# Kernel tuning notes

Hardware: AMD Instinct MI355X
Metric: run time of the kernel (lower is better)

The kernel has to match this reference:

```python
import jax, jax.numpy as jnp
import numpy as np


def setup_inputs() -> dict:
    key = jax.random.key(0)
    k1, k2 = jax.random.split(key)
    B, C, LIN = 8, 128, 65536
    K, LOUT = 9, 16384
    x = jax.random.normal(k1, (B, C, LIN), dtype=jnp.float32)
    neighbours = jax.random.randint(k2, (K, LOUT), 0, LIN, dtype=jnp.int64)
    return {"x": x, "neighbours": neighbours}


def reference(x, neighbours):
    # x: (B, C, locs_in); neighbours: (k, locs_out)
    # gather -> (B, C, k, locs_out), max over k axis -> (B, C, locs_out)
    gathered = x[:, :, neighbours]
    return jnp.max(gathered, axis=-2)
```

## Files before the change

kernel.cpp:

```cpp
#include <hip/hip_runtime.h>
#include <hip/hip_fp16.h>


#define B_DIM 8
#define C_DIM 128
#define LIN 65536
#define K_DIM 9
#define LOUT 16384
#define BC 1024
#define LTILE 16
#define BCCHUNK 256

__global__ __launch_bounds__(256) void transpose_to_half(
    const float4* __restrict__ in4, __half* __restrict__ outh)
{
    __shared__ float tile[64][65];
    const int c0 = blockIdx.x * 64;
    const int r0 = blockIdx.y * 64;
    const int tx = threadIdx.x;
    const int ty = threadIdx.y;

#pragma unroll
    for (int i = 0; i < 4; ++i) {
        const int r = ty + 16 * i;
        const float4 v = in4[(size_t)(r0 + r) * (LIN / 4) + (c0 / 4) + tx];
        tile[r][4 * tx + 0] = v.x;
        tile[r][4 * tx + 1] = v.y;
        tile[r][4 * tx + 2] = v.z;
        tile[r][4 * tx + 3] = v.w;
    }
    __syncthreads();
#pragma unroll
    for (int i = 0; i < 4; ++i) {
        const int c = ty + 16 * i;
        const __half h0 = __float2half_rn(tile[4 * tx + 0][c]);
        const __half h1 = __float2half_rn(tile[4 * tx + 1][c]);
        const __half h2 = __float2half_rn(tile[4 * tx + 2][c]);
        const __half h3 = __float2half_rn(tile[4 * tx + 3][c]);
        ushort4 w;
        w.x = __half_as_ushort(h0);
        w.y = __half_as_ushort(h1);
        w.z = __half_as_ushort(h2);
        w.w = __half_as_ushort(h3);
        *(ushort4*)(outh + (size_t)(c0 + c) * BC + r0 + 4 * tx) = w;
    }
}

__global__ __launch_bounds__(256) void gather_max_half(
    const __half* __restrict__ xTh,
    const int* __restrict__ nbr,
    float* __restrict__ out)
{
    __shared__ float tile[LTILE][BCCHUNK + 4];
    __shared__ int sidx[K_DIM][LTILE];
    const int tid = threadIdx.x;
    const int l0 = blockIdx.x * LTILE;
    const int bc0 = blockIdx.y * BCCHUNK;

    if (tid < K_DIM * LTILE) {
        const int k = tid / LTILE, li = tid % LTILE;
        sidx[k][li] = nbr[k * LOUT + l0 + li];
    }
    __syncthreads();

    const int h = tid & 31;
    const int lgrp = tid >> 5;

#pragma unroll
    for (int j = 0; j < 2; ++j) {
        const int lidx = j * 8 + lgrp;
        float acc[8];
#pragma unroll
        for (int e = 0; e < 8; ++e) acc[e] = -INFINITY;
#pragma unroll
        for (int k = 0; k < K_DIM; ++k) {
            const int id = sidx[k][lidx];
            const float4 raw = *(const float4*)(xTh + (size_t)id * BC + bc0 + 8 * h);
            const __half2* hp = (const __half2*)&raw;
#pragma unroll
            for (int q = 0; q < 4; ++q) {
                const float2 f = __half22float2(hp[q]);
                acc[2 * q]     = fmaxf(acc[2 * q], f.x);
                acc[2 * q + 1] = fmaxf(acc[2 * q + 1], f.y);
            }
        }
        *(float4*)&tile[lidx][8 * h]     = make_float4(acc[0], acc[1], acc[2], acc[3]);
        *(float4*)&tile[lidx][8 * h + 4] = make_float4(acc[4], acc[5], acc[6], acc[7]);
    }
    __syncthreads();

    float* orow = out + (size_t)(bc0 + tid) * LOUT + l0;
#pragma unroll
    for (int j2 = 0; j2 < 4; ++j2) {
        float4 w;
        w.x = tile[4 * j2 + 0][tid];
        w.y = tile[4 * j2 + 1][tid];
        w.z = tile[4 * j2 + 2][tid];
        w.w = tile[4 * j2 + 3][tid];
        *(float4*)(orow + 4 * j2) = w;
    }
}

__global__ __launch_bounds__(256) void pool_gather_max_direct(
    const float* __restrict__ x, const int* __restrict__ nbr, float* __restrict__ out)
{
    const int l = blockIdx.x * 256 + threadIdx.x;
    const int bc0 = blockIdx.y * 8;
    int idx[K_DIM];
#pragma unroll
    for (int k = 0; k < K_DIM; ++k) idx[k] = nbr[k * LOUT + l];
#pragma unroll
    for (int r = 0; r < 8; ++r) {
        const float* __restrict__ xrow = x + (size_t)(bc0 + r) * LIN;
        float m = -INFINITY;
#pragma unroll
        for (int k = 0; k < K_DIM; ++k) m = fmaxf(m, xrow[idx[k]]);
        out[(size_t)(bc0 + r) * LOUT + l] = m;
    }
}

extern "C" void kernel_launch(void* const* d_in, const int* in_sizes, int n_in,
                              void* d_out, int out_size, void* d_ws, size_t ws_size,
                              hipStream_t stream) {
    const float* x   = (const float*)d_in[0];
    const int*   nbr = (const int*)d_in[1];
    float*       out = (float*)d_out;

    const size_t xTh_bytes = (size_t)LIN * BC * sizeof(__half);

    if (ws_size < xTh_bytes) {
        dim3 grid(LOUT / 256, BC / 8);
        pool_gather_max_direct<<<grid, dim3(256), 0, stream>>>(x, nbr, out);
        return;
    }

    __half* xTh = (__half*)d_ws;

    {
        dim3 grid(LIN / 64, BC / 64);
        transpose_to_half<<<grid, dim3(16, 16), 0, stream>>>((const float4*)x, xTh);
    }
    {
        dim3 grid(LOUT / LTILE, BC / BCCHUNK);
        gather_max_half<<<grid, dim3(256), 0, stream>>>(xTh, nbr, out);
    }
}
```

Before: 445.9 us.

## Fuse fp16 conversion and gather-max into per-row kernel using LDS-resident rows

Replaces the global transpose-to-fp16 plus gather kernel with one kernel where each block loads a full (b,c) input row, converts it to fp16 in 128 KB of shared memory, and performs the K-way gather-max from LDS. This removes the intermediate transposed workspace write and read and the scattered global gathers. In exchange, occupancy drops to one large block per CU, load and compute phases do not overlap, and random LDS accesses may bank-conflict. The neighbour indices are re-read by every block, and the low-workspace fallback path is removed.

```diff
diff --git a/kernel.cpp b/kernel.cpp
--- a/kernel.cpp
+++ b/kernel.cpp
@@ -7,141 +7,56 @@
 #define LIN 65536
 #define K_DIM 9
 #define LOUT 16384
-#define BC 1024
-#define LTILE 16
-#define BCCHUNK 256
+#define BC (B_DIM * C_DIM)
+#define NTHREADS 1024
 
-__global__ __launch_bounds__(256) void transpose_to_half(
-    const float4* __restrict__ in4, __half* __restrict__ outh)
-{
-    __shared__ float tile[64][65];
-    const int c0 = blockIdx.x * 64;
-    const int r0 = blockIdx.y * 64;
-    const int tx = threadIdx.x;
-    const int ty = threadIdx.y;
-
-#pragma unroll
-    for (int i = 0; i < 4; ++i) {
-        const int r = ty + 16 * i;
-        const float4 v = in4[(size_t)(r0 + r) * (LIN / 4) + (c0 / 4) + tx];
-        tile[r][4 * tx + 0] = v.x;
-        tile[r][4 * tx + 1] = v.y;
-        tile[r][4 * tx + 2] = v.z;
-        tile[r][4 * tx + 3] = v.w;
-    }
-    __syncthreads();
-#pragma unroll
-    for (int i = 0; i < 4; ++i) {
-        const int c = ty + 16 * i;
-        const __half h0 = __float2half_rn(tile[4 * tx + 0][c]);
-        const __half h1 = __float2half_rn(tile[4 * tx + 1][c]);
-        const __half h2 = __float2half_rn(tile[4 * tx + 2][c]);
-        const __half h3 = __float2half_rn(tile[4 * tx + 3][c]);
-        ushort4 w;
-        w.x = __half_as_ushort(h0);
-        w.y = __half_as_ushort(h1);
-        w.z = __half_as_ushort(h2);
-        w.w = __half_as_ushort(h3);
-        *(ushort4*)(outh + (size_t)(c0 + c) * BC + r0 + 4 * tx) = w;
-    }
-}
-
-__global__ __launch_bounds__(256) void gather_max_half(
-    const __half* __restrict__ xTh,
+__global__ __launch_bounds__(NTHREADS) void fused_rowmax(
+    const float4* __restrict__ x4,
     const int* __restrict__ nbr,
     float* __restrict__ out)
 {
-    __shared__ float tile[LTILE][BCCHUNK + 4];
-    __shared__ int sidx[K_DIM][LTILE];
+    __shared__ __half sh[LIN];
     const int tid = threadIdx.x;
-    const int l0 = blockIdx.x * LTILE;
-    const int bc0 = blockIdx.y * BCCHUNK;
+    const int bc  = blockIdx.x;
 
-    if (tid < K_DIM * LTILE) {
-        const int k = tid / LTILE, li = tid % LTILE;
-        sidx[k][li] = nbr[k * LOUT + l0 + li];
+    const float4* __restrict__ xr = x4 + (size_t)bc * (LIN / 4);
+#pragma unroll
+    for (int r = 0; r < LIN / 4 / NTHREADS; ++r) {
+        const int g = r * NTHREADS + tid;
+        const float4 v = xr[g];
+        ushort4 w;
+        w.x = __half_as_ushort(__float2half_rn(v.x));
+        w.y = __half_as_ushort(__float2half_rn(v.y));
+        w.z = __half_as_ushort(__float2half_rn(v.z));
+        w.w = __half_as_ushort(__float2half_rn(v.w));
+        *(ushort4*)(sh + 4 * g) = w;
     }
     __syncthreads();
 
-    const int h = tid & 31;
-    const int lgrp = tid >> 5;
-
-#pragma unroll
-    for (int j = 0; j < 2; ++j) {
-        const int lidx = j * 8 + lgrp;
-        float acc[8];
-#pragma unroll
-        for (int e = 0; e < 8; ++e) acc[e] = -INFINITY;
+    float* __restrict__ orow = out + (size_t)bc * LOUT;
+#pragma unroll 1
+    for (int it = 0; it < LOUT / (4 * NTHREADS); ++it) {
+        const int l0 = it * (4 * NTHREADS) + 4 * tid;
+        float4 res = make_float4(-INFINITY, -INFINITY, -INFINITY, -INFINITY);
 #pragma unroll
         for (int k = 0; k < K_DIM; ++k) {
-            const int id = sidx[k][lidx];
-            const float4 raw = *(const float4*)(xTh + (size_t)id * BC + bc0 + 8 * h);
-            const __half2* hp = (const __half2*)&raw;
-#pragma unroll
-            for (int q = 0; q < 4; ++q) {
-                const float2 f = __half22float2(hp[q]);
-                acc[2 * q]     = fmaxf(acc[2 * q], f.x);
-                acc[2 * q + 1] = fmaxf(acc[2 * q + 1], f.y);
-            }
+            const int4 id = *(const int4*)(nbr + k * LOUT + l0);
+            res.x = fmaxf(res.x, __half2float(sh[id.x]));
+            res.y = fmaxf(res.y, __half2float(sh[id.y]));
+            res.z = fmaxf(res.z, __half2float(sh[id.z]));
+            res.w = fmaxf(res.w, __half2float(sh[id.w]));
         }
-        *(float4*)&tile[lidx][8 * h]     = make_float4(acc[0], acc[1], acc[2], acc[3]);
-        *(float4*)&tile[lidx][8 * h + 4] = make_float4(acc[4], acc[5], acc[6], acc[7]);
-    }
-    __syncthreads();
-
-    float* orow = out + (size_t)(bc0 + tid) * LOUT + l0;
-#pragma unroll
-    for (int j2 = 0; j2 < 4; ++j2) {
-        float4 w;
-        w.x = tile[4 * j2 + 0][tid];
-        w.y = tile[4 * j2 + 1][tid];
-        w.z = tile[4 * j2 + 2][tid];
-        w.w = tile[4 * j2 + 3][tid];
-        *(float4*)(orow + 4 * j2) = w;
-    }
-}
-
-__global__ __launch_bounds__(256) void pool_gather_max_direct(
-    const float* __restrict__ x, const int* __restrict__ nbr, float* __restrict__ out)
-{
-    const int l = blockIdx.x * 256 + threadIdx.x;
-    const int bc0 = blockIdx.y * 8;
-    int idx[K_DIM];
-#pragma unroll
-    for (int k = 0; k < K_DIM; ++k) idx[k] = nbr[k * LOUT + l];
-#pragma unroll
-    for (int r = 0; r < 8; ++r) {
-        const float* __restrict__ xrow = x + (size_t)(bc0 + r) * LIN;
-        float m = -INFINITY;
-#pragma unroll
-        for (int k = 0; k < K_DIM; ++k) m = fmaxf(m, xrow[idx[k]]);
-        out[(size_t)(bc0 + r) * LOUT + l] = m;
+        *(float4*)(orow + l0) = res;
     }
 }
 
 extern "C" void kernel_launch(void* const* d_in, const int* in_sizes, int n_in,
                               void* d_out, int out_size, void* d_ws, size_t ws_size,
                               hipStream_t stream) {
-    const float* x   = (const float*)d_in[0];
-    const int*   nbr = (const int*)d_in[1];
-    float*       out = (float*)d_out;
+    const float4* x   = (const float4*)d_in[0];
+    const int*    nbr = (const int*)d_in[1];
+    float*        out = (float*)d_out;
+    (void)d_ws; (void)ws_size; (void)in_sizes; (void)n_in; (void)out_size;
 
-    const size_t xTh_bytes = (size_t)LIN * BC * sizeof(__half);
-
-    if (ws_size < xTh_bytes) {
-        dim3 grid(LOUT / 256, BC / 8);
-        pool_gather_max_direct<<<grid, dim3(256), 0, stream>>>(x, nbr, out);
-        return;
-    }
-
-    __half* xTh = (__half*)d_ws;
-
-    {
-        dim3 grid(LIN / 64, BC / 64);
-        transpose_to_half<<<grid, dim3(16, 16), 0, stream>>>((const float4*)x, xTh);
-    }
-    {
-        dim3 grid(LOUT / LTILE, BC / BCCHUNK);
-        gather_max_half<<<grid, dim3(256), 0, stream>>>(xTh, nbr, out);
-    }
+    fused_rowmax<<<dim3(BC), dim3(NTHREADS), 0, stream>>>(x, nbr, out);
 }
```

Measured after the change: 394.2 us. 1.13x faster.
